# Kernel optimization log

Measured on AMD Instinct MI355X. Metric: run time of the kernel, lower is better.

## Reference

```python
import jax, jax.numpy as jnp
import numpy as np

L = 4          # number of Fourier layers
M1, M2 = 16, 16  # retained modes


def setup_inputs() -> dict:
    key = jax.random.key(0)
    ks = jax.random.split(key, 12)
    B, C, H, W = 16, 16, 256, 256
    spec_scale = 1.0 / (C * C)
    return {
        "x": jax.random.normal(ks[0], (B, 1, H, W), jnp.float32),
        "lift_w": jax.random.normal(ks[1], (C, 1), jnp.float32) * 0.5,
        "lift_b": jnp.zeros((C,), jnp.float32),
        "spec_w1r": jax.random.normal(ks[2], (L, C, C, M1, M2), jnp.float32) * spec_scale,
        "spec_w1i": jax.random.normal(ks[3], (L, C, C, M1, M2), jnp.float32) * spec_scale,
        "spec_w2r": jax.random.normal(ks[4], (L, C, C, M1, M2), jnp.float32) * spec_scale,
        "spec_w2i": jax.random.normal(ks[5], (L, C, C, M1, M2), jnp.float32) * spec_scale,
        "skip_w": jax.random.normal(ks[6], (L, C, C), jnp.float32) * (1.0 / np.sqrt(C)),
        "skip_b": jnp.zeros((L, C), jnp.float32),
        "proj_w1": jax.random.normal(ks[7], (128, C), jnp.float32) * (1.0 / np.sqrt(C)),
        "proj_b1": jnp.zeros((128,), jnp.float32),
        "proj_w2": jax.random.normal(ks[8], (64, 128), jnp.float32) * (1.0 / np.sqrt(128)),
        "proj_b2": jnp.zeros((64,), jnp.float32),
        "head_w": jax.random.normal(ks[9], (2, 64), jnp.float32) * (1.0 / np.sqrt(64)),
        "head_b": jnp.zeros((2,), jnp.float32),
    }


def _spectral_conv(v, w1, w2):
    # v: [B,C,H,W] real; w1,w2: [C,C,M1,M2] complex
    B, C, H, W = v.shape
    vft = jnp.fft.rfft2(v)                       # [B,C,H,W//2+1] complex
    top = jnp.einsum('bixy,ioxy->boxy', vft[:, :, :M1, :M2], w1)
    bot = jnp.einsum('bixy,ioxy->boxy', vft[:, :, -M1:, :M2], w2)
    out_ft = jnp.zeros_like(vft)
    out_ft = out_ft.at[:, :, :M1, :M2].set(top)
    out_ft = out_ft.at[:, :, -M1:, :M2].set(bot)
    return jnp.fft.irfft2(out_ft, s=(H, W))


def reference(x, lift_w, lift_b, spec_w1r, spec_w1i, spec_w2r, spec_w2i,
              skip_w, skip_b, proj_w1, proj_b1, proj_w2, proj_b2, head_w, head_b):
    # lifting: 1x1 conv over channels
    v = jnp.einsum('oi,bihw->bohw', lift_w, x) + lift_b[None, :, None, None]
    w1 = spec_w1r + 1j * spec_w1i
    w2 = spec_w2r + 1j * spec_w2i
    for l in range(L):
        sc = _spectral_conv(v, w1[l], w2[l])
        sk = jnp.einsum('oi,bihw->bohw', skip_w[l], v) + skip_b[l][None, :, None, None]
        v = sc + sk
        if l < L - 1:
            v = jax.nn.gelu(v)
    # projection 16 -> 128 -> 64
    q = jax.nn.gelu(jnp.einsum('oi,bihw->bohw', proj_w1, v) + proj_b1[None, :, None, None])
    f = jnp.einsum('oi,bihw->bohw', proj_w2, q) + proj_b2[None, :, None, None]   # [B,64,H,W]
    # head: global avg pool + linear(64,2) + tanh
    pooled = jnp.mean(f, axis=(2, 3))                       # [B,64]
    return jnp.tanh(pooled @ head_w.T + head_b)             # [B,2]
```

## Files before the change

kernel.cpp:

```cpp
#include <hip/hip_runtime.h>
#include <math.h>


#define TWO_PI_OVER_256 0.024543692606170259f

typedef short bf16x8 __attribute__((ext_vector_type(8)));
typedef float f32x4  __attribute__((ext_vector_type(4)));
typedef unsigned int u32;

__device__ __forceinline__ unsigned short bf16_rn(float f){
    unsigned int u = __float_as_uint(f);
    unsigned int r = (u + 0x7fffu + ((u >> 16) & 1u)) >> 16;
    return (unsigned short)r;
}
__device__ __forceinline__ float bf16_tf(unsigned short h){
    return __uint_as_float(((unsigned int)h) << 16);
}
__device__ __forceinline__ u32 pack_hilo(float f){
    unsigned short hi = bf16_rn(f);
    unsigned short lo = bf16_rn(f - bf16_tf(hi));
    return (u32)hi | ((u32)lo << 16);
}

__device__ __forceinline__ float gelu_f(float x){
    float x2 = x*x;
    float z2 = x*(1.5957691f + 0.07135482f*x2);
    float e = __expf(-z2);
    return x * __builtin_amdgcn_rcpf(1.0f + e);
}

__device__ __forceinline__ void build_tables(float* s_c, float* s_s){
    int t = threadIdx.x;
    if(t < 256){
        float ang = (float)t * TWO_PI_OVER_256;
        float sv, cv;
        sincosf(ang, &sv, &cv);
        s_c[t] = cv; s_s[t] = sv;
    }
}

__device__ __forceinline__ float2 dft_row(const float* s_row, const float* s_c, const float* s_s, int ky){
    float stc = s_c[(4*ky)&255], sts = s_s[(4*ky)&255];
    float rc = 1.0f, rs = 0.0f;
    float accR[4] = {0,0,0,0}, accI[4] = {0,0,0,0};
    const float4* row4 = (const float4*)s_row;
    #pragma unroll 4
    for(int m=0;m<64;m++){
        float4 v4 = row4[m];
        accR[0]+=v4.x*rc; accI[0]+=v4.x*rs;
        accR[1]+=v4.y*rc; accI[1]+=v4.y*rs;
        accR[2]+=v4.z*rc; accI[2]+=v4.z*rs;
        accR[3]+=v4.w*rc; accI[3]+=v4.w*rs;
        float nr = rc*stc + rs*sts;
        float ni = rs*stc - rc*sts;
        rc=nr; rs=ni;
    }
    float oR=0.0f, oI=0.0f;
    #pragma unroll
    for(int j=0;j<4;j++){
        float cj = s_c[(ky*j)&255], sj = s_s[(ky*j)&255];
        oR += accR[j]*cj + accI[j]*sj;
        oI += accI[j]*cj - accR[j]*sj;
    }
    return make_float2(oR, oI);
}

__global__ __launch_bounds__(256) void fno_zero_k(float* __restrict__ p, int n){
    int i = blockIdx.x*256 + threadIdx.x;
    if(i < n) p[i] = 0.0f;
}

__global__ __launch_bounds__(256) void fno_wprep_k(const float* __restrict__ w1r, const float* __restrict__ w1i,
                                                   const float* __restrict__ w2r, const float* __restrict__ w2i,
                                                   float2* __restrict__ Wt2){
    int lin = blockIdx.x;
    int l  = lin >> 9;
    int rem = lin & 511;
    int o = rem >> 5;
    int kxIdx = rem & 31;
    int t = threadIdx.x;
    int ky = t >> 4, i = t & 15;
    int x = kxIdx & 15;
    const float* wr = (kxIdx < 16) ? w1r : w2r;
    const float* wi = (kxIdx < 16) ? w1i : w2i;
    int src = (((l*16 + i)*16 + o)*16 + x)*16 + ky;
    Wt2[((size_t)(l*16 + o)*512 + kxIdx*16 + ky)*16 + i] = make_float2(wr[src], wi[src]);
}

__global__ __launch_bounds__(256) void fno_tabs_k(const float* __restrict__ skw, const float* __restrict__ W1,
                                                  unsigned short* __restrict__ Ep, unsigned short* __restrict__ Fp,
                                                  unsigned short* __restrict__ skA, unsigned short* __restrict__ W1A){
    int idx = blockIdx.x*256 + threadIdx.x;
    if(idx < 16384){
        int rem = idx;
        int pass = rem >> 13; rem &= 8191;
        int nt = rem >> 9; rem &= 511;
        int quad = rem >> 7;
        int col = (rem >> 3) & 15;
        int j = rem & 7;
        int k = quad*8 + j;
        int ky = k >> 1, ri = k & 1;
        int w = nt*16 + col;
        int ph = (ky*w) & 255;
        float sv, cv; sincosf((float)ph * TWO_PI_OVER_256, &sv, &cv);
        float val = ri ? -sv : cv;
        unsigned short hi = bf16_rn(val);
        Ep[idx] = pass ? bf16_rn(val - bf16_tf(hi)) : hi;
    } else if(idx < 16384 + 32768){
        int rem = idx - 16384;
        int pass = rem >> 14; rem &= 16383;
        int nt2 = rem >> 13; rem &= 8191;
        int s = rem >> 9; rem &= 511;
        int quad = rem >> 7;
        int col = (rem >> 3) & 15;
        int j = rem & 7;
        int wp = s*16 + quad*4 + (j >> 1);
        int kyRI = nt2*16 + col;
        int ky = kyRI >> 1, ri = kyRI & 1;
        int ph = (ky*wp) & 255;
        float sv, cv; sincosf((float)ph * TWO_PI_OVER_256, &sv, &cv);
        float val = ri ? -sv : cv;
        unsigned short hi = bf16_rn(val);
        Fp[idx - 16384] = pass ? bf16_rn(val - bf16_tf(hi)) : hi;
    } else if(idx < 16384 + 32768 + 4096){
        int rem = idx - (16384 + 32768);
        int l = rem >> 10;
        int part = (rem >> 9) & 1;
        int quad = (rem >> 7) & 3;
        int col = (rem >> 3) & 15;
        int j = rem & 7;
        int c = quad*4 + (j >> 1);
        float wv = skw[(l*16 + col)*16 + c];
        unsigned short hi = bf16_rn(wv);
        skA[rem] = part ? bf16_rn(wv - bf16_tf(hi)) : hi;
    } else if(idx < 16384 + 32768 + 4096 + 4096){
        int rem = idx - (16384 + 32768 + 4096);
        int kt = rem >> 9;
        int quad = (rem >> 7) & 3;
        int col = (rem >> 3) & 15;
        int j = rem & 7;
        float wv = W1[(kt*16 + col)*16 + (quad & 1)*8 + j];
        unsigned short hi = bf16_rn(wv);
        W1A[rem] = (quad >> 1) ? bf16_rn(wv - bf16_tf(hi)) : hi;
    }
}

__global__ __launch_bounds__(256) void fno_liftf1_k(const float* __restrict__ x, const float* __restrict__ lw,
                                                    const float* __restrict__ lb, u32* __restrict__ vp,
                                                    float2* __restrict__ Fw){
    __shared__ float s_v[16*260];
    __shared__ float s_c[256], s_s[256];
    int t = threadIdx.x;
    build_tables(s_c, s_s);
    int b = blockIdx.x >> 8, h = blockIdx.x & 255;
    float xv = x[(b*256 + h)*256 + t];
    #pragma unroll
    for(int c=0;c<16;c++){
        float val = lw[c]*xv + lb[c];
        s_v[c*260 + t] = val;
    }
    __syncthreads();
    uint4* vp4 = (uint4*)(vp + (size_t)(b*256 + h)*4096);
    #pragma unroll
    for(int it=0;it<4;it++){
        int idx = it*256 + t;
        int px = idx >> 2, sg = idx & 3;
        int cg = sg ^ ((px >> 2) & 3);
        uint4 pk;
        pk.x = pack_hilo(s_v[(cg*4+0)*260 + px]);
        pk.y = pack_hilo(s_v[(cg*4+1)*260 + px]);
        pk.z = pack_hilo(s_v[(cg*4+2)*260 + px]);
        pk.w = pack_hilo(s_v[(cg*4+3)*260 + px]);
        vp4[idx] = pk;
    }
    int c = t >> 4, ky = t & 15;
    float2 r = dft_row(s_v + c*260, s_c, s_s, ky);
    Fw[((size_t)(b*16 + c)*256 + h)*16 + ky] = r;
}

__global__ __launch_bounds__(256) void fno_f2q_k(const float2* __restrict__ Fw, float2* __restrict__ vftp){
    __shared__ float2 s_fw[1024];
    __shared__ float2 s_red[2048];
    __shared__ float s_c[256], s_s[256];
    int t = threadIdx.x;
    build_tables(s_c, s_s);
    int bc = blockIdx.x >> 2, qr = blockIdx.x & 3;
    int qh = qr*64;
    {
        const float4* src = (const float4*)(Fw + (size_t)bc*4096 + qh*16);
        float4* d4 = (float4*)s_fw;
        for(int i=t;i<512;i+=256) d4[i] = src[i];
    }
    __syncthreads();
    int sub = t>>6, kyp = (t>>3)&7, kxg = t&7;
    int h0 = qh + sub*16;
    float rc[4], rs[4], stc[4], sts[4], aR[4][2], aI[4][2];
    #pragma unroll
    for(int p=0;p<4;p++){
        int kxIdx = kxg*4+p;
        int kx = kxIdx + ((kxIdx>=16)?224:0);
        int i0 = (kx*h0)&255;
        rc[p] = s_c[i0]; rs[p] = -s_s[i0];
        stc[p] = s_c[kx]; sts[p] = s_s[kx];
        aR[p][0]=aR[p][1]=aI[p][0]=aI[p][1]=0.0f;
    }
    #pragma unroll 4
    for(int hh=0; hh<16; hh++){
        float4 f = *(const float4*)&s_fw[(sub*16 + hh)*16 + kyp*2];
        #pragma unroll
        for(int p=0;p<4;p++){
            aR[p][0] += f.x*rc[p] - f.y*rs[p];
            aI[p][0] += f.x*rs[p] + f.y*rc[p];
            aR[p][1] += f.z*rc[p] - f.w*rs[p];
            aI[p][1] += f.z*rs[p] + f.w*rc[p];
            float nr = rc[p]*stc[p] + rs[p]*sts[p];
            float ni = rs[p]*stc[p] - rc[p]*sts[p];
            rc[p]=nr; rs[p]=ni;
        }
    }
    #pragma unroll
    for(int p=0;p<4;p++)
        #pragma unroll
        for(int y=0;y<2;y++)
            s_red[sub*512 + (kxg*4+p)*16 + kyp*2 + y] = make_float2(aR[p][y], aI[p][y]);
    __syncthreads();
    #pragma unroll
    for(int u=0;u<2;u++){
        int oidx = t*2 + u;
        float xr=0.0f, xi=0.0f;
        #pragma unroll
        for(int q=0;q<4;q++){ float2 pr = s_red[q*512 + oidx]; xr += pr.x; xi += pr.y; }
        vftp[(size_t)blockIdx.x*512 + oidx] = make_float2(xr, xi);
    }
}

__global__ __launch_bounds__(256) void fno_mixi1_k(const float2* __restrict__ vftp, const float2* __restrict__ Wt2,
                                                   float2* __restrict__ Gh, int l){
    __shared__ float2 s_oft[512];
    __shared__ float s_c[256], s_s[256];
    int t = threadIdx.x;
    build_tables(s_c, s_s);
    int b = blockIdx.x >> 4, o = blockIdx.x & 15;
    const float2* vb = vftp + (size_t)b*16*2048;
    const float2* wb = Wt2 + (size_t)(l*16 + o)*512*16;
    #pragma unroll
    for(int u=0;u<2;u++){
        int m = t + u*256;
        const float2* wm = wb + m*16;
        float aR=0.0f, aI=0.0f;
        #pragma unroll
        for(int i=0;i<16;i++){
            const float2* q0 = vb + i*2048 + m;
            float2 a0 = q0[0], a1 = q0[512], a2 = q0[1024], a3 = q0[1536];
            float vxr = a0.x+a1.x+a2.x+a3.x;
            float vxi = a0.y+a1.y+a2.y+a3.y;
            float2 wv = wm[i];
            aR += vxr*wv.x - vxi*wv.y;
            aI += vxr*wv.y + vxi*wv.x;
        }
        s_oft[m] = make_float2(aR, aI);
    }
    __syncthreads();
    int h = t;
    float hc = s_c[h], hs = s_s[h];
    float aR[16], aI[16];
    #pragma unroll
    for(int ky=0;ky<16;ky++){ aR[ky]=0.0f; aI[ky]=0.0f; }
    float rc = 1.0f, rs = 0.0f;
    for(int kxIdx=0;kxIdx<16;kxIdx++){
        #pragma unroll
        for(int ky=0;ky<16;ky++){
            float2 g = s_oft[kxIdx*16 + ky];
            aR[ky] += g.x*rc - g.y*rs;
            aI[ky] += g.x*rs + g.y*rc;
        }
        float nr = rc*hc - rs*hs, ni = rc*hs + rs*hc;
        rc=nr; rs=ni;
    }
    { int i0 = (240*h)&255; rc = s_c[i0]; rs = s_s[i0]; }
    for(int kxIdx=16;kxIdx<32;kxIdx++){
        #pragma unroll
        for(int ky=0;ky<16;ky++){
            float2 g = s_oft[kxIdx*16 + ky];
            aR[ky] += g.x*rc - g.y*rs;
            aI[ky] += g.x*rs + g.y*rc;
        }
        float nr = rc*hc - rs*hs, ni = rc*hs + rs*hc;
        rc=nr; rs=ni;
    }
    const float inv = 1.0f/65536.0f;
    float4 pack[8];
    #pragma unroll
    for(int ky=0;ky<16;ky+=2){
        float s0 = (ky==0) ? inv : 2.0f*inv;
        float s1 = 2.0f*inv;
        pack[ky/2] = make_float4(aR[ky]*s0, aI[ky]*s0, aR[ky+1]*s1, aI[ky+1]*s1);
    }
    float4* d4 = (float4*)(Gh + ((size_t)(b*256 + h)*16 + o)*16);
    #pragma unroll
    for(int q=0;q<8;q++) d4[q] = pack[q];
}

__device__ __forceinline__ bf16x8 load_G_hi(const float2* __restrict__ Gh, int b, int h,
                                            int quad, int col){
    const float* gp = (const float*)Gh + (size_t)(b*256 + h)*512 + col*32 + quad*8;
    float4 g0 = *(const float4*)gp;
    float4 g1 = *(const float4*)(gp + 4);
    float g[8] = {g0.x,g0.y,g0.z,g0.w,g1.x,g1.y,g1.z,g1.w};
    bf16x8 ghi;
    #pragma unroll
    for(int j=0;j<8;j++) ghi[j] = (short)bf16_rn(g[j]);
    return ghi;
}

__global__ __launch_bounds__(256, 3) void fno_layer_k(const float2* __restrict__ Gh, u32* __restrict__ vp,
                                                      const unsigned short* __restrict__ Ep,
                                                      const unsigned short* __restrict__ Fp,
                                                      const unsigned short* __restrict__ skA,
                                                      const float* __restrict__ skb,
                                                      float2* __restrict__ Fw, int l){
    __shared__ u32 s_hilo[16*260];
    __shared__ float s_part[8*64*4];
    int t = threadIdx.x;
    int wave = t >> 6, lane = t & 63, quad = lane >> 4, col = lane & 15;
    int b = blockIdx.x >> 6, hg = blockIdx.x & 63;

    bf16x8 a_whi = *(const bf16x8*)&skA[((l*2 + 0)*64 + lane)*8];
    float4 skb4 = *(const float4*)&skb[l*16 + quad*4];
    float bv[4] = {skb4.x, skb4.y, skb4.z, skb4.w};
    int qs = quad ^ ((col >> 2) & 3);

    for(int hi2=0; hi2<4; hi2++){
        int h = hg*4 + hi2;
        u32* vpb = vp + (size_t)(b*256 + h)*4096;
        bf16x8 ghi = load_G_hi(Gh, b, h, quad, col);
        #pragma unroll
        for(int i=0;i<4;i++){
            int nt = wave*4 + i;
            int w = nt*16 + col;
            bf16x8 bskip = *(const bf16x8*)&vpb[w*16 + qs*4];
            bf16x8 behi = *(const bf16x8*)&Ep[((0*16 + nt)*64 + lane)*8];
            f32x4 acc = {0.0f,0.0f,0.0f,0.0f};
            acc = __builtin_amdgcn_mfma_f32_16x16x32_bf16(a_whi, bskip, acc, 0,0,0);
            acc = __builtin_amdgcn_mfma_f32_16x16x32_bf16(ghi, behi, acc, 0,0,0);
            uint4 pk;
            u32* pkp = (u32*)&pk;
            #pragma unroll
            for(int r=0;r<4;r++){
                float val = gelu_f(acc[r] + bv[r]);
                int o = quad*4 + r;
                u32 p = pack_hilo(val);
                s_hilo[o*260 + w] = p;
                pkp[r] = p;
            }
            *(uint4*)&vpb[w*16 + qs*4] = pk;
        }
        __syncthreads();
        f32x4 facc[2];
        facc[0] = (f32x4){0,0,0,0}; facc[1] = (f32x4){0,0,0,0};
        #pragma unroll
        for(int si=0;si<4;si++){
            int s = wave*4 + si;
            bf16x8 af = *(const bf16x8*)&s_hilo[col*260 + s*16 + quad*4];
            #pragma unroll
            for(int nt2=0;nt2<2;nt2++){
                bf16x8 bhi = *(const bf16x8*)&Fp[(((0*2 + nt2)*16 + s)*64 + lane)*8];
                facc[nt2] = __builtin_amdgcn_mfma_f32_16x16x32_bf16(af, bhi, facc[nt2], 0,0,0);
            }
        }
        #pragma unroll
        for(int nt2=0;nt2<2;nt2++){
            float4 fv = {facc[nt2][0], facc[nt2][1], facc[nt2][2], facc[nt2][3]};
            *(float4*)&s_part[((wave*2 + nt2)*64 + lane)*4] = fv;
        }
        __syncthreads();
        {
            int c = t >> 4, jj = t & 15;
            int nt2 = jj >> 3, kyl = jj & 7;
            int ky = nt2*8 + kyl;
            int lidx = (c >> 2)*16 + kyl*2;
            int reg = c & 3;
            float re = 0.0f, im = 0.0f;
            #pragma unroll
            for(int wv=0;wv<4;wv++){
                re += s_part[((wv*2 + nt2)*64 + lidx)*4 + reg];
                im += s_part[((wv*2 + nt2)*64 + lidx + 1)*4 + reg];
            }
            Fw[((size_t)(b*16 + c)*256 + h)*16 + ky] = make_float2(re, im);
        }
    }
}

__global__ __launch_bounds__(256) void fno_l3proj_k(const float2* __restrict__ Gh, const u32* __restrict__ vp,
                                                    const unsigned short* __restrict__ Ep,
                                                    const unsigned short* __restrict__ skA,
                                                    const float* __restrict__ skb,
                                                    const unsigned short* __restrict__ W1A,
                                                    const float* __restrict__ b1,
                                                    float* __restrict__ poolq){
    __shared__ unsigned short s_b2[4096];
    __shared__ float s_b1[128];
    __shared__ float s_red[128*5];
    int t = threadIdx.x;
    int wave = t >> 6, lane = t & 63, quad = lane >> 4, col = lane & 15;
    int b = blockIdx.x >> 6, hg = blockIdx.x & 63;

    if(t < 128) s_b1[t] = b1[t];
    bf16x8 a_whi = *(const bf16x8*)&skA[((3*2 + 0)*64 + lane)*8];
    float4 skb4 = *(const float4*)&skb[3*16 + quad*4];
    float bv[4] = {skb4.x, skb4.y, skb4.z, skb4.w};
    int qs = quad ^ ((col >> 2) & 3);
    __syncthreads();

    float pacc[8][4];
    #pragma unroll
    for(int kt=0;kt<8;kt++)
        #pragma unroll
        for(int r=0;r<4;r++) pacc[kt][r] = 0.0f;

    for(int hi2=0; hi2<4; hi2++){
        int h = hg*4 + hi2;
        const u32* vpb = vp + (size_t)(b*256 + h)*4096;
        bf16x8 ghi = load_G_hi(Gh, b, h, quad, col);
        #pragma unroll
        for(int i=0;i<4;i++){
            int nt = wave*4 + i;
            int w = nt*16 + col;
            bf16x8 bskip = *(const bf16x8*)&vpb[w*16 + qs*4];
            bf16x8 behi = *(const bf16x8*)&Ep[((0*16 + nt)*64 + lane)*8];
            f32x4 acc = {0.0f,0.0f,0.0f,0.0f};
            acc = __builtin_amdgcn_mfma_f32_16x16x32_bf16(a_whi, bskip, acc, 0,0,0);
            acc = __builtin_amdgcn_mfma_f32_16x16x32_bf16(ghi, behi, acc, 0,0,0);
            #pragma unroll
            for(int r=0;r<2;r++){
                u32 p = (u32)bf16_rn(acc[2*r] + bv[2*r]) | ((u32)bf16_rn(acc[2*r+1] + bv[2*r+1]) << 16);
                *(u32*)&s_b2[w*16 + quad*4 + 2*r] = p;
            }
        }
        bf16x8 bfrag[4];
        #pragma unroll
        for(int i=0;i<4;i++){
            int wt = wave*4 + i;
            bfrag[i] = *(const bf16x8*)&s_b2[(wt*16 + col)*16 + (quad & 1)*8];
        }
        #pragma unroll
        for(int kt=0;kt<8;kt++){
            bf16x8 w1 = *(const bf16x8*)&W1A[(kt*64 + lane)*8];
            float4 bias = *(const float4*)&s_b1[kt*16 + quad*4];
            #pragma unroll
            for(int i=0;i<4;i++){
                f32x4 d = {0.0f,0.0f,0.0f,0.0f};
                d = __builtin_amdgcn_mfma_f32_16x16x32_bf16(w1, bfrag[i], d, 0,0,0);
                pacc[kt][0] += gelu_f(d[0] + bias.x);
                pacc[kt][1] += gelu_f(d[1] + bias.y);
                pacc[kt][2] += gelu_f(d[2] + bias.z);
                pacc[kt][3] += gelu_f(d[3] + bias.w);
            }
        }
    }
    #pragma unroll
    for(int kt=0;kt<8;kt++){
        #pragma unroll
        for(int r=0;r<4;r++){
            float s = pacc[kt][r];
            s += __shfl_xor(s, 1);
            s += __shfl_xor(s, 2);
            s += __shfl_xor(s, 4);
            s += __shfl_xor(s, 8);
            if(col == 0) s_red[(kt*16 + quad*4 + r)*5 + wave] = s;
        }
    }
    __syncthreads();
    if(t < 128){
        float s = s_red[t*5+0] + s_red[t*5+1] + s_red[t*5+2] + s_red[t*5+3];
        atomicAdd(&poolq[b*128 + t], s);
    }
}

__global__ __launch_bounds__(1024) void fno_head_k(const float* __restrict__ poolq, const float* __restrict__ W2,
                                                   const float* __restrict__ b2, const float* __restrict__ hw,
                                                   const float* __restrict__ hb, float* __restrict__ out){
    __shared__ float s_pool[16][68];
    int t = threadIdx.x;
    int b = t >> 6, j = t & 63;
    const float* pq = poolq + b*128;
    const float* w2 = W2 + j*128;
    float dot = 0.0f;
    for(int k=0;k<128;k++) dot += w2[k]*pq[k];
    s_pool[b][j] = b2[j] + dot*(1.0f/65536.0f);
    __syncthreads();
    if(t < 32){
        int bb = t >> 1, c2 = t & 1;
        float z = hb[c2];
        #pragma unroll
        for(int j2=0;j2<64;j2++) z += hw[c2*64 + j2]*s_pool[bb][j2];
        out[bb*2 + c2] = tanhf(z);
    }
}

extern "C" void kernel_launch(void* const* d_in, const int* in_sizes, int n_in,
                              void* d_out, int out_size, void* d_ws, size_t ws_size,
                              hipStream_t stream) {
    const float* x       = (const float*)d_in[0];
    const float* lift_w  = (const float*)d_in[1];
    const float* lift_b  = (const float*)d_in[2];
    const float* w1r     = (const float*)d_in[3];
    const float* w1i     = (const float*)d_in[4];
    const float* w2r     = (const float*)d_in[5];
    const float* w2i     = (const float*)d_in[6];
    const float* skip_w  = (const float*)d_in[7];
    const float* skip_b  = (const float*)d_in[8];
    const float* proj_w1 = (const float*)d_in[9];
    const float* proj_b1 = (const float*)d_in[10];
    const float* proj_w2 = (const float*)d_in[11];
    const float* proj_b2 = (const float*)d_in[12];
    const float* head_w  = (const float*)d_in[13];
    const float* head_b  = (const float*)d_in[14];
    float* out = (float*)d_out;

    u32*    vp   = (u32*)d_ws;
    float2* Fw   = (float2*)(vp + 16777216);
    float2* vftp = Fw  + 1048576;
    float2* Gh   = vftp + 524288;
    float2* Wt2  = Gh  + 1048576;
    float*  poolq = (float*)(Wt2 + 524288);
    unsigned short* Ep  = (unsigned short*)(poolq + 2048);
    unsigned short* Fp  = Ep + 16384;
    unsigned short* skA = Fp + 32768;
    unsigned short* W1A = skA + 4096;

    fno_zero_k<<<8, 256, 0, stream>>>(poolq, 2048);
    fno_wprep_k<<<2048, 256, 0, stream>>>(w1r, w1i, w2r, w2i, Wt2);
    fno_tabs_k<<<224, 256, 0, stream>>>(skip_w, proj_w1, Ep, Fp, skA, W1A);
    fno_liftf1_k<<<4096, 256, 0, stream>>>(x, lift_w, lift_b, vp, Fw);

    for(int l=0; l<4; l++){
        fno_f2q_k<<<1024, 256, 0, stream>>>(Fw, vftp);
        fno_mixi1_k<<<256, 256, 0, stream>>>(vftp, Wt2, Gh, l);
        if(l < 3){
            fno_layer_k<<<1024, 256, 0, stream>>>(Gh, vp, Ep, Fp, skA, skip_b, Fw, l);
        } else {
            fno_l3proj_k<<<1024, 256, 0, stream>>>(Gh, vp, Ep, skA, skip_b, W1A, proj_b1, poolq);
        }
    }

    fno_head_k<<<1, 1024, 0, stream>>>(poolq, proj_w2, proj_b2, head_w, head_b, out);
}
```

Before: 420.6 us.

## Split spectral mixing across ky halves and defer layer partial reductions

fno_mixi1_k now splits each (batch, output channel) block into two ky halves. This doubles the grid to 512 blocks and halves the per-thread accumulator arrays, giving more parallelism and lower register pressure. fno_layer_k drops the per-row block barriers: the s_hilo exchange stays within one wave, and partial Fourier sums for all four rows are kept in a larger shared buffer and reduced after a single barrier. The trade-off is roughly double the shared memory per block and removal of the 3-blocks-per-CU launch bound hint, which may lower occupancy.

After: 402.1 us. 4.4% less time.

```diff
diff --git a/kernel.cpp b/kernel.cpp
--- a/kernel.cpp
+++ b/kernel.cpp
@@ -236,16 +236,18 @@
 
 __global__ __launch_bounds__(256) void fno_mixi1_k(const float2* __restrict__ vftp, const float2* __restrict__ Wt2,
                                                    float2* __restrict__ Gh, int l){
-    __shared__ float2 s_oft[512];
+    __shared__ float2 s_oft[256];
     __shared__ float s_c[256], s_s[256];
     int t = threadIdx.x;
     build_tables(s_c, s_s);
-    int b = blockIdx.x >> 4, o = blockIdx.x & 15;
+    int b = blockIdx.x >> 5;
+    int o = (blockIdx.x >> 1) & 15;
+    int kyh = blockIdx.x & 1;
     const float2* vb = vftp + (size_t)b*16*2048;
     const float2* wb = Wt2 + (size_t)(l*16 + o)*512*16;
-    #pragma unroll
-    for(int u=0;u<2;u++){
-        int m = t + u*256;
+    {
+        int kx = t >> 3, kyl = t & 7;
+        int m = kx*16 + kyh*8 + kyl;
         const float2* wm = wb + m*16;
         float aR=0.0f, aI=0.0f;
         #pragma unroll
@@ -258,21 +260,21 @@
             aR += vxr*wv.x - vxi*wv.y;
             aI += vxr*wv.y + vxi*wv.x;
         }
-        s_oft[m] = make_float2(aR, aI);
+        s_oft[t] = make_float2(aR, aI);
     }
     __syncthreads();
     int h = t;
     float hc = s_c[h], hs = s_s[h];
-    float aR[16], aI[16];
-    #pragma unroll
-    for(int ky=0;ky<16;ky++){ aR[ky]=0.0f; aI[ky]=0.0f; }
+    float aR[8], aI[8];
+    #pragma unroll
+    for(int q=0;q<8;q++){ aR[q]=0.0f; aI[q]=0.0f; }
     float rc = 1.0f, rs = 0.0f;
     for(int kxIdx=0;kxIdx<16;kxIdx++){
         #pragma unroll
-        for(int ky=0;ky<16;ky++){
-            float2 g = s_oft[kxIdx*16 + ky];
-            aR[ky] += g.x*rc - g.y*rs;
-            aI[ky] += g.x*rs + g.y*rc;
+        for(int q=0;q<8;q++){
+            float2 g = s_oft[kxIdx*8 + q];
+            aR[q] += g.x*rc - g.y*rs;
+            aI[q] += g.x*rs + g.y*rc;
         }
         float nr = rc*hc - rs*hs, ni = rc*hs + rs*hc;
         rc=nr; rs=ni;
@@ -280,25 +282,25 @@
     { int i0 = (240*h)&255; rc = s_c[i0]; rs = s_s[i0]; }
     for(int kxIdx=16;kxIdx<32;kxIdx++){
         #pragma unroll
-        for(int ky=0;ky<16;ky++){
-            float2 g = s_oft[kxIdx*16 + ky];
-            aR[ky] += g.x*rc - g.y*rs;
-            aI[ky] += g.x*rs + g.y*rc;
+        for(int q=0;q<8;q++){
+            float2 g = s_oft[kxIdx*8 + q];
+            aR[q] += g.x*rc - g.y*rs;
+            aI[q] += g.x*rs + g.y*rc;
         }
         float nr = rc*hc - rs*hs, ni = rc*hs + rs*hc;
         rc=nr; rs=ni;
     }
     const float inv = 1.0f/65536.0f;
-    float4 pack[8];
-    #pragma unroll
-    for(int ky=0;ky<16;ky+=2){
-        float s0 = (ky==0) ? inv : 2.0f*inv;
+    float4 pack[4];
+    #pragma unroll
+    for(int q=0;q<8;q+=2){
+        float s0 = (kyh==0 && q==0) ? inv : 2.0f*inv;
         float s1 = 2.0f*inv;
-        pack[ky/2] = make_float4(aR[ky]*s0, aI[ky]*s0, aR[ky+1]*s1, aI[ky+1]*s1);
-    }
-    float4* d4 = (float4*)(Gh + ((size_t)(b*256 + h)*16 + o)*16);
-    #pragma unroll
-    for(int q=0;q<8;q++) d4[q] = pack[q];
+        pack[q/2] = make_float4(aR[q]*s0, aI[q]*s0, aR[q+1]*s1, aI[q+1]*s1);
+    }
+    float4* d4 = (float4*)(Gh + ((size_t)(b*256 + h)*16 + o)*16 + kyh*8);
+    #pragma unroll
+    for(int q=0;q<4;q++) d4[q] = pack[q];
 }
 
 __device__ __forceinline__ bf16x8 load_G_hi(const float2* __restrict__ Gh, int b, int h,
@@ -313,14 +315,14 @@
     return ghi;
 }
 
-__global__ __launch_bounds__(256, 3) void fno_layer_k(const float2* __restrict__ Gh, u32* __restrict__ vp,
-                                                      const unsigned short* __restrict__ Ep,
-                                                      const unsigned short* __restrict__ Fp,
-                                                      const unsigned short* __restrict__ skA,
-                                                      const float* __restrict__ skb,
-                                                      float2* __restrict__ Fw, int l){
+__global__ __launch_bounds__(256) void fno_layer_k(const float2* __restrict__ Gh, u32* __restrict__ vp,
+                                                   const unsigned short* __restrict__ Ep,
+                                                   const unsigned short* __restrict__ Fp,
+                                                   const unsigned short* __restrict__ skA,
+                                                   const float* __restrict__ skb,
+                                                   float2* __restrict__ Fw, int l){
     __shared__ u32 s_hilo[16*260];
-    __shared__ float s_part[8*64*4];
+    __shared__ float s_part4[4*2048];
     int t = threadIdx.x;
     int wave = t >> 6, lane = t & 63, quad = lane >> 4, col = lane & 15;
     int b = blockIdx.x >> 6, hg = blockIdx.x & 63;
@@ -355,7 +357,6 @@
             }
             *(uint4*)&vpb[w*16 + qs*4] = pk;
         }
-        __syncthreads();
         f32x4 facc[2];
         facc[0] = (f32x4){0,0,0,0}; facc[1] = (f32x4){0,0,0,0};
         #pragma unroll
@@ -371,22 +372,25 @@
         #pragma unroll
         for(int nt2=0;nt2<2;nt2++){
             float4 fv = {facc[nt2][0], facc[nt2][1], facc[nt2][2], facc[nt2][3]};
-            *(float4*)&s_part[((wave*2 + nt2)*64 + lane)*4] = fv;
-        }
-        __syncthreads();
-        {
-            int c = t >> 4, jj = t & 15;
-            int nt2 = jj >> 3, kyl = jj & 7;
-            int ky = nt2*8 + kyl;
-            int lidx = (c >> 2)*16 + kyl*2;
-            int reg = c & 3;
+            *(float4*)&s_part4[hi2*2048 + ((wave*2 + nt2)*64 + lane)*4] = fv;
+        }
+    }
+    __syncthreads();
+    {
+        int c = t >> 4, jj = t & 15;
+        int nt2 = jj >> 3, kyl = jj & 7;
+        int ky = nt2*8 + kyl;
+        int lidx = (c >> 2)*16 + kyl*2;
+        int reg = c & 3;
+        #pragma unroll
+        for(int hi2=0;hi2<4;hi2++){
             float re = 0.0f, im = 0.0f;
             #pragma unroll
             for(int wv=0;wv<4;wv++){
-                re += s_part[((wv*2 + nt2)*64 + lidx)*4 + reg];
-                im += s_part[((wv*2 + nt2)*64 + lidx + 1)*4 + reg];
+                re += s_part4[hi2*2048 + ((wv*2 + nt2)*64 + lidx)*4 + reg];
+                im += s_part4[hi2*2048 + ((wv*2 + nt2)*64 + lidx + 1)*4 + reg];
             }
-            Fw[((size_t)(b*16 + c)*256 + h)*16 + ky] = make_float2(re, im);
+            Fw[((size_t)(b*16 + c)*256 + hg*4 + hi2)*16 + ky] = make_float2(re, im);
         }
     }
 }
@@ -536,7 +540,7 @@
 
     for(int l=0; l<4; l++){
         fno_f2q_k<<<1024, 256, 0, stream>>>(Fw, vftp);
-        fno_mixi1_k<<<256, 256, 0, stream>>>(vftp, Wt2, Gh, l);
+        fno_mixi1_k<<<512, 256, 0, stream>>>(vftp, Wt2, Gh, l);
         if(l < 3){
             fno_layer_k<<<1024, 256, 0, stream>>>(Gh, vp, Ep, Fp, skA, skip_b, Fw, l);
         } else {
```
